# Kernel tuning notes

Measured on AMD Instinct MI355X. Metric: run time of the kernel, lower is better.

## Reference

```python
import jax, jax.numpy as jnp
import numpy as np

B, L, DIM, H = 2, 2048, 1024, 16
HD = DIM // H  # 64
EPS = 1e-6
ROPE_THETA = 10000.0


def _rmsnorm(x, scale):
    # mean of squares in float32 as in torch (dtype=torch.float32)
    ms = jnp.mean(jnp.square(x.astype(jnp.float32)), axis=-1, keepdims=True)
    inv = jax.lax.rsqrt(ms + EPS).astype(x.dtype)
    return x * inv * scale.astype(x.dtype)


def _rope_cos_sin(seq_len, head_dim, dtype):
    inv_freq = 1.0 / (ROPE_THETA ** (jnp.arange(0, head_dim, 2, dtype=jnp.float32) / head_dim))
    ang = jnp.arange(seq_len, dtype=jnp.float32)[:, None] * inv_freq[None, :]  # [L, HD/2]
    cos = jnp.cos(ang)[:, None, :].astype(dtype)  # [L,1,HD/2] broadcast over heads
    sin = jnp.sin(ang)[:, None, :].astype(dtype)
    return cos, sin


def _rope_apply(x, cos, sin):
    # x: [B,L,H,HD]; rotate-half formulation
    x1, x2 = jnp.split(x, 2, axis=-1)
    return jnp.concatenate([x1 * cos - x2 * sin, x2 * cos + x1 * sin], axis=-1)


def setup_inputs() -> dict:
    key = jax.random.key(0)
    k1, k2, k3 = jax.random.split(key, 3)
    x = jax.random.normal(k1, (B, L, DIM), dtype=jnp.float32)
    Wqkv = jax.random.normal(k2, (DIM, 3 * DIM), dtype=jnp.float32) * (DIM ** -0.5)
    Wproj = jax.random.normal(k3, (DIM, DIM), dtype=jnp.float32) * (DIM ** -0.5)
    q_scale = jnp.ones((HD,), dtype=jnp.float32)
    k_scale = jnp.ones((HD,), dtype=jnp.float32)
    bproj = jnp.zeros((DIM,), dtype=jnp.float32)
    return {"x": x, "Wqkv": Wqkv, "q_scale": q_scale, "k_scale": k_scale,
            "Wproj": Wproj, "bproj": bproj}


def reference(x, Wqkv, q_scale, k_scale, Wproj, bproj):
    b, l, c = x.shape
    qkv = x @ Wqkv  # [B,L,3*DIM]
    qkv = qkv.reshape(b, l, 3, H, HD)
    q, k, v = qkv[:, :, 0], qkv[:, :, 1], qkv[:, :, 2]  # each [B,L,H,HD]
    q = _rmsnorm(q, q_scale)
    k = _rmsnorm(k, k_scale)
    cos, sin = _rope_cos_sin(l, HD, x.dtype)
    q = _rope_apply(q, cos, sin)
    k = _rope_apply(k, cos, sin)
    scale = HD ** -0.5
    scores = jnp.einsum('blhd,bmhd->bhlm', q, k) * scale  # [B,H,L,L]
    p = jax.nn.softmax(scores, axis=-1)
    o = jnp.einsum('bhlm,bmhd->blhd', p, v).reshape(b, l, c)
    return o @ Wproj + bproj
```

## Files before the change

kernel.cpp:

```cpp
#include <hip/hip_runtime.h>
#include <hip/hip_bf16.h>
#include <cstdint>

#define B_   2
#define L_   2048
#define DIM_ 1024
#define H_   16
#define HD_  64
#define M_   (B_ * L_)
#define N3_  (3 * DIM_)

typedef unsigned short ushort_t;
typedef __bf16 bf16x8 __attribute__((ext_vector_type(8)));
typedef float  f32x4  __attribute__((ext_vector_type(4)));
typedef float  f32x16 __attribute__((ext_vector_type(16)));
typedef unsigned u32x2_t __attribute__((ext_vector_type(2)));

__device__ __forceinline__ unsigned short f2b(float f) {
  return __builtin_bit_cast(unsigned short, (__bf16)f);
}
__device__ __forceinline__ float b2f(unsigned short s) {
  unsigned u = ((unsigned)s) << 16;
  return __builtin_bit_cast(float, u);
}
__device__ __forceinline__ float fmax3(float a, float b, float c) {
  return fmaxf(fmaxf(a, b), c);
}

__device__ __forceinline__ void plswap(unsigned &a, unsigned &b) {
#if defined(__has_builtin) && __has_builtin(__builtin_amdgcn_permlane32_swap)
  u32x2_t r = __builtin_amdgcn_permlane32_swap(a, b, false, false);
  a = r[0]; b = r[1];
#else
  unsigned sa = (unsigned)__shfl_xor((int)a, 32);
  unsigned sb = (unsigned)__shfl_xor((int)b, 32);
  bool hi = (threadIdx.x & 32) != 0;
  unsigned na = hi ? sb : a;
  unsigned nb = hi ? b : sa;
  a = na; b = nb;
#endif
}

typedef const __attribute__((address_space(1))) void* as1cp;
typedef __attribute__((address_space(3))) void* as3p;
__device__ __forceinline__ void gload_lds16(const void* g, void* l) {
  __builtin_amdgcn_global_load_lds((as1cp)g, (as3p)l, 16, 0, 0);
}

__global__ __launch_bounds__(256)
void conv_bf16(const float* __restrict__ in, ushort_t* __restrict__ out, int n4) {
  int i = blockIdx.x * 256 + threadIdx.x;
  if (i >= n4) return;
  float4 v = *(const float4*)&in[(size_t)i * 4];
  ushort4 o;
  o.x = f2b(v.x); o.y = f2b(v.y); o.z = f2b(v.z); o.w = f2b(v.w);
  *(ushort4*)&out[(size_t)i * 4] = o;
}

__global__ __launch_bounds__(256)
void transpose_conv(const float* __restrict__ in, ushort_t* __restrict__ out,
                    int R, int C) {
  __shared__ float tile[64][65];
  const int t = threadIdx.x;
  const int r0 = blockIdx.y * 64, c0 = blockIdx.x * 64;
#pragma unroll
  for (int p = 0; p < 4; ++p) {
    int r = (t >> 4) + p * 16;
    int c = (t & 15) * 4;
    float4 v = *(const float4*)&in[(size_t)(r0 + r) * C + (c0 + c)];
    tile[r][c + 0] = v.x; tile[r][c + 1] = v.y;
    tile[r][c + 2] = v.z; tile[r][c + 3] = v.w;
  }
  __syncthreads();
#pragma unroll
  for (int p = 0; p < 4; ++p) {
    int cc = (t >> 4) + p * 16;
    int r  = (t & 15) * 4;
    ushort4 o;
    o.x = f2b(tile[r + 0][cc]); o.y = f2b(tile[r + 1][cc]);
    o.z = f2b(tile[r + 2][cc]); o.w = f2b(tile[r + 3][cc]);
    *(ushort4*)&out[(size_t)(c0 + cc) * R + (r0 + r)] = o;
  }
}

__global__ __launch_bounds__(256)
void rope_tab(float* __restrict__ cosT, float* __restrict__ sinT) {
  int idx = blockIdx.x * 256 + threadIdx.x;
  int l = idx >> 5, d = idx & 31;
  float inv_freq = expf(-((float)(2 * d) / 64.f) * logf(10000.f));
  float ang = (float)l * inv_freq;
  cosT[idx] = cosf(ang);
  sinT[idx] = sinf(ang);
}

template <int MODE>
__global__ __launch_bounds__(256)
void gemm_bt(const ushort_t* __restrict__ A, const ushort_t* __restrict__ BT,
             void* __restrict__ Cout, ushort_t* __restrict__ vtout,
             const float* __restrict__ bias, int M, int N, int K, int ldc) {
  __shared__ ushort_t As[128 * 32];
  __shared__ ushort_t Bs[128 * 32];
  const int lane = threadIdx.x & 63;
  const int wid  = threadIdx.x >> 6;
  const int wm = wid >> 1, wn = wid & 1;
  const int m0 = blockIdx.y * 128, n0 = blockIdx.x * 128;
  const int ro = lane & 15, kg = lane >> 4;

  f32x4 acc[4][4] = {};

  for (int k0 = 0; k0 < K; k0 += 32) {
    const int cb = wid * 128;
#pragma unroll
    for (int j = 0; j < 2; ++j) {
      int c = cb + j * 64 + lane;
      gload_lds16(A + (size_t)(m0 + (c >> 2)) * K + k0 + (c & 3) * 8,
                  &As[(cb + j * 64) * 8]);
    }
#pragma unroll
    for (int j = 0; j < 2; ++j) {
      int c = cb + j * 64 + lane;
      gload_lds16(BT + (size_t)(n0 + (c >> 2)) * K + k0 + (c & 3) * 8,
                  &Bs[(cb + j * 64) * 8]);
    }
    __syncthreads();
    bf16x8 af[4], bfr[4];
#pragma unroll
    for (int i = 0; i < 4; ++i)
      af[i] = *(const bf16x8*)&As[(wm * 64 + i * 16 + ro) * 32 + kg * 8];
#pragma unroll
    for (int i = 0; i < 4; ++i)
      bfr[i] = *(const bf16x8*)&Bs[(wn * 64 + i * 16 + ro) * 32 + kg * 8];
#pragma unroll
    for (int i = 0; i < 4; ++i)
#pragma unroll
      for (int j = 0; j < 4; ++j)
        acc[i][j] = __builtin_amdgcn_mfma_f32_16x16x32_bf16(af[i], bfr[j],
                                                            acc[i][j], 0, 0, 0);
    __syncthreads();
  }

  if (MODE == 0) {
    if (n0 < 2048) {
#pragma unroll
      for (int i = 0; i < 4; ++i)
#pragma unroll
        for (int r = 0; r < 4; ++r) {
          int row = m0 + wm * 64 + i * 16 + kg * 4 + r;
#pragma unroll
          for (int j = 0; j < 4; ++j) {
            int col = n0 + wn * 64 + j * 16 + ro;
            ((ushort_t*)Cout)[(size_t)row * ldc + col] = f2b(acc[i][j][r]);
          }
        }
    } else {
#pragma unroll
      for (int i = 0; i < 4; ++i) {
        int rowb = m0 + wm * 64 + i * 16 + kg * 4;
        int bb = rowb >> 11, l = rowb & (L_ - 1);
#pragma unroll
        for (int j = 0; j < 4; ++j) {
          int dg = (n0 - 2048) + wn * 64 + j * 16 + ro;
          ushort4 o;
          o.x = f2b(acc[i][j][0]); o.y = f2b(acc[i][j][1]);
          o.z = f2b(acc[i][j][2]); o.w = f2b(acc[i][j][3]);
          *(ushort4*)&vtout[((size_t)bb * DIM_ + dg) * L_ + l] = o;
        }
      }
    }
  } else {
#pragma unroll
    for (int i = 0; i < 4; ++i)
#pragma unroll
      for (int r = 0; r < 4; ++r) {
        int row = m0 + wm * 64 + i * 16 + kg * 4 + r;
#pragma unroll
        for (int j = 0; j < 4; ++j) {
          int col = n0 + wn * 64 + j * 16 + ro;
          ((float*)Cout)[(size_t)row * ldc + col] = acc[i][j][r] + bias[col];
        }
      }
  }
}

__global__ __launch_bounds__(256)
void rmsrope(ushort_t* __restrict__ qk, const float* __restrict__ qs,
             const float* __restrict__ ks, const float* __restrict__ cosT,
             const float* __restrict__ sinT) {
  const int t = blockIdx.x;
  const int l = t & (L_ - 1);
  const int j = threadIdx.x & 15;
  const int h = threadIdx.x >> 4;
  const int dd = (j & 7) * 4;
  float4 cv = *(const float4*)&cosT[l * 32 + dd];
  float4 sv = *(const float4*)&sinT[l * 32 + dd];
  const float sgn = (j < 8) ? -1.f : 1.f;
#pragma unroll
  for (int ic = 0; ic < 2; ++ic) {
    const float qsc = (ic == 0) ? 0.125f * 1.44269504088896341f : 1.f;
    ushort_t* base = qk + (size_t)t * 2048 + ic * DIM_ + h * HD_ + j * 4;
    ushort4 raw = *(const ushort4*)base;
    float x0 = b2f(raw.x), x1 = b2f(raw.y), x2 = b2f(raw.z), x3 = b2f(raw.w);
    float ss = x0 * x0 + x1 * x1 + x2 * x2 + x3 * x3;
    ss += __shfl_xor(ss, 1); ss += __shfl_xor(ss, 2);
    ss += __shfl_xor(ss, 4); ss += __shfl_xor(ss, 8);
    float inv = rsqrtf(ss * (1.f / 64.f) + 1e-6f);
    const float* scp = (ic == 0 ? qs : ks) + j * 4;
    float4 sc = *(const float4*)scp;
    x0 *= inv * sc.x; x1 *= inv * sc.y; x2 *= inv * sc.z; x3 *= inv * sc.w;
    float y0 = __shfl_xor(x0, 8), y1 = __shfl_xor(x1, 8);
    float y2 = __shfl_xor(x2, 8), y3 = __shfl_xor(x3, 8);
    ushort4 o;
    o.x = f2b((x0 * cv.x + sgn * y0 * sv.x) * qsc);
    o.y = f2b((x1 * cv.y + sgn * y1 * sv.y) * qsc);
    o.z = f2b((x2 * cv.z + sgn * y2 * sv.z) * qsc);
    o.w = f2b((x3 * cv.w + sgn * y3 * sv.w) * qsc);
    *(ushort4*)base = o;
  }
}

__global__ __launch_bounds__(256)
void flash_attn(const ushort_t* __restrict__ qk, const ushort_t* __restrict__ vt,
                ushort_t* __restrict__ O) {
  const int qt = blockIdx.x, h = blockIdx.y, b = blockIdx.z;
  const int lane = threadIdx.x & 63, wid = threadIdx.x >> 6;
  const int lq = lane & 31;
  const int hi = lane >> 5;
  const int q0 = qt * 128;
  const size_t tok0 = (size_t)b * L_;
  const ushort_t* qb = qk + tok0 * 2048 + h * HD_;
  const ushort_t* kb = qb + DIM_;
  const ushort_t* vb = vt + ((size_t)b * DIM_ + h * HD_) * L_;

  __shared__ ushort_t Ks[2][4096];
  __shared__ ushort_t Vs[2][4096];

  const int srow0 = wid * 16 + (lane >> 3);
  const int sch   = lane & 7;
  auto STAGE = [&](int bufi, int kt) {
#pragma unroll
    for (int j = 0; j < 2; ++j) {
      int row = srow0 + j * 8;
      int sc  = sch ^ (row & 7);
      gload_lds16(kb + (size_t)(kt * 64 + row) * 2048 + sc * 8,
                  &Ks[bufi][wid * 1024 + j * 512]);
      gload_lds16(vb + (size_t)row * L_ + kt * 64 + sc * 8,
                  &Vs[bufi][wid * 1024 + j * 512]);
    }
  };

  bf16x8 qf[4];
  {
    const ushort_t* gp = qb + (size_t)(q0 + wid * 32 + lq) * 2048;
#pragma unroll
    for (int s = 0; s < 4; ++s)
      qf[s] = *(const bf16x8*)(gp + s * 16 + hi * 8);
  }

  int chs[4];
#pragma unroll
  for (int s = 0; s < 4; ++s) chs[s] = ((2 * s + hi) ^ (lq & 7)) * 8;

  f32x16 oaccT[2] = {};
  float mrow = -1e30f, lrow = 0.f;

  STAGE(0, 0);
  __syncthreads();

  auto TILE = [&](int bi, int kt) {
    if (kt + 1 < L_ / 64) STAGE(bi ^ 1, kt + 1);
    const ushort_t* kb0 = &Ks[bi][lq * 64];
    const ushort_t* vb0 = &Vs[bi][lq * 64];

    f32x16 st[2];
    __builtin_amdgcn_s_setprio(1);
#pragma unroll
    for (int t = 0; t < 2; ++t) {
      f32x16 z = {};
#pragma unroll
      for (int s = 0; s < 4; ++s) {
        bf16x8 kf = *(const bf16x8*)(kb0 + t * 2048 + chs[s]);
        z = __builtin_amdgcn_mfma_f32_32x32x16_bf16(kf, qf[s], z, 0, 0, 0);
      }
      st[t] = z;
    }
    __builtin_amdgcn_s_setprio(0);

    float mx0, mx1, mx2, mx3;
    {
      float a0 = fmaxf(fmaxf(st[0][0], st[0][1]),  fmaxf(st[0][2], st[0][3]));
      float a1 = fmaxf(fmaxf(st[0][4], st[0][5]),  fmaxf(st[0][6], st[0][7]));
      float a2 = fmaxf(fmaxf(st[0][8], st[0][9]),  fmaxf(st[0][10], st[0][11]));
      float a3 = fmaxf(fmaxf(st[0][12], st[0][13]), fmaxf(st[0][14], st[0][15]));
      float b0 = fmaxf(fmaxf(st[1][0], st[1][1]),  fmaxf(st[1][2], st[1][3]));
      float b1 = fmaxf(fmaxf(st[1][4], st[1][5]),  fmaxf(st[1][6], st[1][7]));
      float b2 = fmaxf(fmaxf(st[1][8], st[1][9]),  fmaxf(st[1][10], st[1][11]));
      float b3 = fmaxf(fmaxf(st[1][12], st[1][13]), fmaxf(st[1][14], st[1][15]));
      mx0 = fmaxf(a0, b0); mx1 = fmaxf(a1, b1);
      mx2 = fmaxf(a2, b2); mx3 = fmaxf(a3, b3);
    }
    float pmw = fmaxf(fmax3(mx0, mx1, mx2), mx3);
    float pm  = fmaxf(pmw, __shfl_xor(pmw, 32));

    if (__any(pm > mrow + 8.f)) {
      float mn = fmaxf(mrow, pm);
      float alpha = __builtin_amdgcn_exp2f(mrow - mn);
      mrow = mn;
      lrow *= alpha;
#pragma unroll
      for (int dt = 0; dt < 2; ++dt)
#pragma unroll
        for (int r = 0; r < 16; ++r) oaccT[dt][r] *= alpha;
    }

    unsigned pk[2][8];
    float rs0 = 0.f, rs1 = 0.f, rs2 = 0.f, rs3 = 0.f;
#pragma unroll
    for (int t = 0; t < 2; ++t)
#pragma unroll
      for (int p = 0; p < 8; ++p) {
        float e0 = __builtin_amdgcn_exp2f(st[t][2 * p]     - mrow);
        float e1 = __builtin_amdgcn_exp2f(st[t][2 * p + 1] - mrow);
        if ((p & 3) == 0) { rs0 += e0; rs1 += e1; }
        else if ((p & 3) == 1) { rs2 += e0; rs3 += e1; }
        else if ((p & 3) == 2) { rs0 += e0; rs1 += e1; }
        else { rs2 += e0; rs3 += e1; }
        pk[t][p] = (unsigned)f2b(e0) | ((unsigned)f2b(e1) << 16);
      }
    lrow += (rs0 + rs1) + (rs2 + rs3);

    __builtin_amdgcn_s_setprio(1);
#pragma unroll
    for (int t = 0; t < 2; ++t)
#pragma unroll
      for (int blk = 0; blk < 2; ++blk) {
        unsigned w0 = pk[t][4 * blk + 0], w1 = pk[t][4 * blk + 1];
        unsigned w2 = pk[t][4 * blk + 2], w3 = pk[t][4 * blk + 3];
        plswap(w0, w2);
        plswap(w1, w3);
        uint4 bw; bw.x = w0; bw.y = w1; bw.z = w2; bw.w = w3;
        bf16x8 pf = __builtin_bit_cast(bf16x8, bw);
        const int sg = 2 * t + blk;
#pragma unroll
        for (int dt = 0; dt < 2; ++dt) {
          bf16x8 vf = *(const bf16x8*)(vb0 + dt * 2048 + chs[sg]);
          oaccT[dt] = __builtin_amdgcn_mfma_f32_32x32x16_bf16(vf, pf,
                                                              oaccT[dt], 0, 0, 0);
        }
      }
    __builtin_amdgcn_s_setprio(0);

    __syncthreads();
  };

  for (int kt = 0; kt < L_ / 64; kt += 2) {
    TILE(0, kt);
    TILE(1, kt + 1);
  }

  lrow += __shfl_xor(lrow, 32);
  float linv = 1.f / lrow;
  ushort_t* obp = O + (size_t)(tok0 + q0 + wid * 32 + lq) * DIM_ + h * HD_;
#pragma unroll
  for (int dt = 0; dt < 2; ++dt)
#pragma unroll
    for (int g4 = 0; g4 < 4; ++g4) {
      int d0 = dt * 32 + g4 * 8 + hi * 4;
      ushort4 o4;
      o4.x = f2b(oaccT[dt][4 * g4 + 0] * linv);
      o4.y = f2b(oaccT[dt][4 * g4 + 1] * linv);
      o4.z = f2b(oaccT[dt][4 * g4 + 2] * linv);
      o4.w = f2b(oaccT[dt][4 * g4 + 3] * linv);
      *(ushort4*)(obp + d0) = o4;
    }
}

extern "C" void kernel_launch(void* const* d_in, const int* in_sizes, int n_in,
                              void* d_out, int out_size, void* d_ws, size_t ws_size,
                              hipStream_t stream) {
  const float* x     = (const float*)d_in[0];
  const float* Wqkv  = (const float*)d_in[1];
  const float* qs    = (const float*)d_in[2];
  const float* ks    = (const float*)d_in[3];
  const float* Wproj = (const float*)d_in[4];
  const float* bproj = (const float*)d_in[5];
  float* out = (float*)d_out;

  char* ws = (char*)d_ws;
  ushort_t* xb     = (ushort_t*)(ws);
  ushort_t* WqkvT  = (ushort_t*)(ws + (size_t)(8u << 20));
  ushort_t* WprojT = (ushort_t*)(ws + (size_t)(14u << 20));
  ushort_t* qkb    = (ushort_t*)(ws + (size_t)(16u << 20));
  ushort_t* vtb    = (ushort_t*)(ws + (size_t)(32u << 20));
  float*    cosT   = (float*)(ws + (size_t)(40u << 20));
  float*    sinT   = (float*)(ws + (size_t)(40u << 20) + (256u << 10));
  ushort_t* ob     = (ushort_t*)(ws + (size_t)(41u << 20));

  conv_bf16<<<4096, 256, 0, stream>>>(x, xb, M_ * DIM_ / 4);
  transpose_conv<<<dim3(48, 16), 256, 0, stream>>>(Wqkv, WqkvT, DIM_, N3_);
  transpose_conv<<<dim3(16, 16), 256, 0, stream>>>(Wproj, WprojT, DIM_, DIM_);
  rope_tab<<<256, 256, 0, stream>>>(cosT, sinT);
  gemm_bt<0><<<dim3(24, 32), 256, 0, stream>>>(xb, WqkvT, qkb, vtb, nullptr,
                                               M_, N3_, DIM_, 2048);
  rmsrope<<<4096, 256, 0, stream>>>(qkb, qs, ks, cosT, sinT);
  flash_attn<<<dim3(16, 16, 2), 256, 0, stream>>>(qkb, vtb, ob);
  gemm_bt<1><<<dim3(8, 32), 256, 0, stream>>>(ob, WprojT, out, nullptr, bproj,
                                              M_, DIM_, DIM_, DIM_);
}
```

Before: 151.3 us.

## Split flash attention over KV halves with combine kernel and MFMA row sums

Flash attention now splits the key/value sequence into two halves via a SPLIT template, doubling the grid from 512 to 1024 blocks so more of the 256 CUs are busy. Each half writes fp32 partial outputs plus per-row max and sum to workspace, and a new attn_combine kernel merges them into the bf16 output. The softmax row sum is now accumulated with an extra MFMA against a ones vector rather than scalar adds, and the max reduction is restructured around fmax3. The cost is an extra launch and fp32 partial-output traffic, and the split path runs only when the workspace is large enough.

```diff
diff --git a/kernel.cpp b/kernel.cpp
--- a/kernel.cpp
+++ b/kernel.cpp
@@ -218,10 +218,16 @@
   }
 }
 
+template <int SPLIT>
 __global__ __launch_bounds__(256)
 void flash_attn(const ushort_t* __restrict__ qk, const ushort_t* __restrict__ vt,
-                ushort_t* __restrict__ O) {
-  const int qt = blockIdx.x, h = blockIdx.y, b = blockIdx.z;
+                ushort_t* __restrict__ O, float* __restrict__ Opart,
+                float* __restrict__ Ml) {
+  const int qt = blockIdx.x, h = blockIdx.y;
+  const int b  = SPLIT ? (int)(blockIdx.z >> 1) : (int)blockIdx.z;
+  const int ks = SPLIT ? (int)(blockIdx.z & 1) : 0;
+  const int ktBeg = SPLIT ? ks * (L_ / 128) : 0;
+  const int ktEnd = SPLIT ? ktBeg + (L_ / 128) : (L_ / 64);
   const int lane = threadIdx.x & 63, wid = threadIdx.x >> 6;
   const int lq = lane & 31;
   const int hi = lane >> 5;
@@ -256,18 +262,23 @@
       qf[s] = *(const bf16x8*)(gp + s * 16 + hi * 8);
   }
 
+  bf16x8 onesv;
+#pragma unroll
+  for (int i = 0; i < 8; ++i) onesv[i] = (__bf16)1.0f;
+
   int chs[4];
 #pragma unroll
   for (int s = 0; s < 4; ++s) chs[s] = ((2 * s + hi) ^ (lq & 7)) * 8;
 
   f32x16 oaccT[2] = {};
-  float mrow = -1e30f, lrow = 0.f;
-
-  STAGE(0, 0);
+  f32x16 laccv = {};
+  float mrow = -1e30f;
+
+  STAGE(0, ktBeg);
   __syncthreads();
 
   auto TILE = [&](int bi, int kt) {
-    if (kt + 1 < L_ / 64) STAGE(bi ^ 1, kt + 1);
+    if (kt + 1 < ktEnd) STAGE(bi ^ 1, kt + 1);
     const ushort_t* kb0 = &Ks[bi][lq * 64];
     const ushort_t* vb0 = &Vs[bi][lq * 64];
 
@@ -285,27 +296,29 @@
     }
     __builtin_amdgcn_s_setprio(0);
 
-    float mx0, mx1, mx2, mx3;
-    {
-      float a0 = fmaxf(fmaxf(st[0][0], st[0][1]),  fmaxf(st[0][2], st[0][3]));
-      float a1 = fmaxf(fmaxf(st[0][4], st[0][5]),  fmaxf(st[0][6], st[0][7]));
-      float a2 = fmaxf(fmaxf(st[0][8], st[0][9]),  fmaxf(st[0][10], st[0][11]));
-      float a3 = fmaxf(fmaxf(st[0][12], st[0][13]), fmaxf(st[0][14], st[0][15]));
-      float b0 = fmaxf(fmaxf(st[1][0], st[1][1]),  fmaxf(st[1][2], st[1][3]));
-      float b1 = fmaxf(fmaxf(st[1][4], st[1][5]),  fmaxf(st[1][6], st[1][7]));
-      float b2 = fmaxf(fmaxf(st[1][8], st[1][9]),  fmaxf(st[1][10], st[1][11]));
-      float b3 = fmaxf(fmaxf(st[1][12], st[1][13]), fmaxf(st[1][14], st[1][15]));
-      mx0 = fmaxf(a0, b0); mx1 = fmaxf(a1, b1);
-      mx2 = fmaxf(a2, b2); mx3 = fmaxf(a3, b3);
-    }
-    float pmw = fmaxf(fmax3(mx0, mx1, mx2), mx3);
+    float m01 = fmax3(st[0][0],  st[0][1],  st[0][2]);
+    float m02 = fmax3(st[0][3],  st[0][4],  st[0][5]);
+    float m03 = fmax3(st[0][6],  st[0][7],  st[0][8]);
+    float m04 = fmax3(st[0][9],  st[0][10], st[0][11]);
+    float m05 = fmax3(st[0][12], st[0][13], st[0][14]);
+    float m06 = fmax3(st[0][15], st[1][0],  st[1][1]);
+    float m07 = fmax3(st[1][2],  st[1][3],  st[1][4]);
+    float m08 = fmax3(st[1][5],  st[1][6],  st[1][7]);
+    float m09 = fmax3(st[1][8],  st[1][9],  st[1][10]);
+    float m10 = fmax3(st[1][11], st[1][12], st[1][13]);
+    float m11 = fmaxf(st[1][14], st[1][15]);
+    float n1 = fmax3(m01, m02, m03);
+    float n2 = fmax3(m04, m05, m06);
+    float n3 = fmax3(m07, m08, m09);
+    float n4 = fmax3(m10, m11, n1);
+    float pmw = fmax3(n2, n3, n4);
     float pm  = fmaxf(pmw, __shfl_xor(pmw, 32));
 
     if (__any(pm > mrow + 8.f)) {
       float mn = fmaxf(mrow, pm);
       float alpha = __builtin_amdgcn_exp2f(mrow - mn);
       mrow = mn;
-      lrow *= alpha;
+      laccv[0] *= alpha;
 #pragma unroll
       for (int dt = 0; dt < 2; ++dt)
 #pragma unroll
@@ -313,20 +326,14 @@
     }
 
     unsigned pk[2][8];
-    float rs0 = 0.f, rs1 = 0.f, rs2 = 0.f, rs3 = 0.f;
 #pragma unroll
     for (int t = 0; t < 2; ++t)
 #pragma unroll
       for (int p = 0; p < 8; ++p) {
         float e0 = __builtin_amdgcn_exp2f(st[t][2 * p]     - mrow);
         float e1 = __builtin_amdgcn_exp2f(st[t][2 * p + 1] - mrow);
-        if ((p & 3) == 0) { rs0 += e0; rs1 += e1; }
-        else if ((p & 3) == 1) { rs2 += e0; rs3 += e1; }
-        else if ((p & 3) == 2) { rs0 += e0; rs1 += e1; }
-        else { rs2 += e0; rs3 += e1; }
         pk[t][p] = (unsigned)f2b(e0) | ((unsigned)f2b(e1) << 16);
       }
-    lrow += (rs0 + rs1) + (rs2 + rs3);
 
     __builtin_amdgcn_s_setprio(1);
 #pragma unroll
@@ -340,6 +347,7 @@
         uint4 bw; bw.x = w0; bw.y = w1; bw.z = w2; bw.w = w3;
         bf16x8 pf = __builtin_bit_cast(bf16x8, bw);
         const int sg = 2 * t + blk;
+        laccv = __builtin_amdgcn_mfma_f32_32x32x16_bf16(onesv, pf, laccv, 0, 0, 0);
 #pragma unroll
         for (int dt = 0; dt < 2; ++dt) {
           bf16x8 vf = *(const bf16x8*)(vb0 + dt * 2048 + chs[sg]);
@@ -352,26 +360,72 @@
     __syncthreads();
   };
 
-  for (int kt = 0; kt < L_ / 64; kt += 2) {
+  for (int kt = ktBeg; kt < ktEnd; kt += 2) {
     TILE(0, kt);
     TILE(1, kt + 1);
   }
 
-  lrow += __shfl_xor(lrow, 32);
-  float linv = 1.f / lrow;
-  ushort_t* obp = O + (size_t)(tok0 + q0 + wid * 32 + lq) * DIM_ + h * HD_;
-#pragma unroll
-  for (int dt = 0; dt < 2; ++dt)
-#pragma unroll
-    for (int g4 = 0; g4 < 4; ++g4) {
-      int d0 = dt * 32 + g4 * 8 + hi * 4;
-      ushort4 o4;
-      o4.x = f2b(oaccT[dt][4 * g4 + 0] * linv);
-      o4.y = f2b(oaccT[dt][4 * g4 + 1] * linv);
-      o4.z = f2b(oaccT[dt][4 * g4 + 2] * linv);
-      o4.w = f2b(oaccT[dt][4 * g4 + 3] * linv);
-      *(ushort4*)(obp + d0) = o4;
-    }
+  const float linv = 1.f / laccv[0];
+  const int tok = (int)tok0 + q0 + wid * 32 + lq;
+  if (SPLIT) {
+    float* op = Opart + ((size_t)ks * M_ + tok) * DIM_ + h * HD_;
+#pragma unroll
+    for (int dt = 0; dt < 2; ++dt)
+#pragma unroll
+      for (int g4 = 0; g4 < 4; ++g4) {
+        int d0 = dt * 32 + g4 * 8 + hi * 4;
+        float4 o4;
+        o4.x = oaccT[dt][4 * g4 + 0] * linv;
+        o4.y = oaccT[dt][4 * g4 + 1] * linv;
+        o4.z = oaccT[dt][4 * g4 + 2] * linv;
+        o4.w = oaccT[dt][4 * g4 + 3] * linv;
+        *(float4*)(op + d0) = o4;
+      }
+    if (hi == 0) {
+      float2 ml; ml.x = mrow; ml.y = laccv[0];
+      *(float2*)&Ml[(((size_t)ks * M_ + tok) * H_ + h) * 2] = ml;
+    }
+  } else {
+    ushort_t* obp = O + (size_t)tok * DIM_ + h * HD_;
+#pragma unroll
+    for (int dt = 0; dt < 2; ++dt)
+#pragma unroll
+      for (int g4 = 0; g4 < 4; ++g4) {
+        int d0 = dt * 32 + g4 * 8 + hi * 4;
+        ushort4 o4;
+        o4.x = f2b(oaccT[dt][4 * g4 + 0] * linv);
+        o4.y = f2b(oaccT[dt][4 * g4 + 1] * linv);
+        o4.z = f2b(oaccT[dt][4 * g4 + 2] * linv);
+        o4.w = f2b(oaccT[dt][4 * g4 + 3] * linv);
+        *(ushort4*)(obp + d0) = o4;
+      }
+  }
+}
+
+__global__ __launch_bounds__(256)
+void attn_combine(const float* __restrict__ Opart, const float* __restrict__ Ml,
+                  ushort_t* __restrict__ O) {
+  int idx = blockIdx.x * 256 + threadIdx.x;
+  int dg  = idx & 15;
+  int rest = idx >> 4;
+  int h   = rest & 15;
+  int tok = rest >> 4;
+  float2 ml0 = *(const float2*)&Ml[(((size_t)0 * M_ + tok) * H_ + h) * 2];
+  float2 ml1 = *(const float2*)&Ml[(((size_t)1 * M_ + tok) * H_ + h) * 2];
+  float mM = fmaxf(ml0.x, ml1.x);
+  float w0 = ml0.y * __builtin_amdgcn_exp2f(ml0.x - mM);
+  float w1 = ml1.y * __builtin_amdgcn_exp2f(ml1.x - mM);
+  float inv = 1.f / (w0 + w1);
+  w0 *= inv; w1 *= inv;
+  size_t off = (size_t)tok * DIM_ + h * HD_ + dg * 4;
+  float4 a = *(const float4*)&Opart[off];
+  float4 c = *(const float4*)&Opart[(size_t)M_ * DIM_ + off];
+  ushort4 o;
+  o.x = f2b(a.x * w0 + c.x * w1);
+  o.y = f2b(a.y * w0 + c.y * w1);
+  o.z = f2b(a.z * w0 + c.z * w1);
+  o.w = f2b(a.w * w0 + c.w * w1);
+  *(ushort4*)&O[off] = o;
 }
 
 extern "C" void kernel_launch(void* const* d_in, const int* in_sizes, int n_in,
@@ -394,6 +448,8 @@
   float*    cosT   = (float*)(ws + (size_t)(40u << 20));
   float*    sinT   = (float*)(ws + (size_t)(40u << 20) + (256u << 10));
   ushort_t* ob     = (ushort_t*)(ws + (size_t)(41u << 20));
+  float*    Opart  = (float*)(ws + (size_t)(49u << 20));
+  float*    Ml     = (float*)(ws + (size_t)(81u << 20));
 
   conv_bf16<<<4096, 256, 0, stream>>>(x, xb, M_ * DIM_ / 4);
   transpose_conv<<<dim3(48, 16), 256, 0, stream>>>(Wqkv, WqkvT, DIM_, N3_);
@@ -402,7 +458,14 @@
   gemm_bt<0><<<dim3(24, 32), 256, 0, stream>>>(xb, WqkvT, qkb, vtb, nullptr,
                                                M_, N3_, DIM_, 2048);
   rmsrope<<<4096, 256, 0, stream>>>(qkb, qs, ks, cosT, sinT);
-  flash_attn<<<dim3(16, 16, 2), 256, 0, stream>>>(qkb, vtb, ob);
+  if (ws_size >= ((size_t)83u << 20)) {
+    flash_attn<1><<<dim3(16, 16, 4), 256, 0, stream>>>(qkb, vtb, nullptr,
+                                                       Opart, Ml);
+    attn_combine<<<4096, 256, 0, stream>>>(Opart, Ml, ob);
+  } else {
+    flash_attn<0><<<dim3(16, 16, 2), 256, 0, stream>>>(qkb, vtb, ob,
+                                                       nullptr, nullptr);
+  }
   gemm_bt<1><<<dim3(8, 32), 256, 0, stream>>>(ob, WprojT, out, nullptr, bproj,
                                               M_, DIM_, DIM_, DIM_);
 }
```

Result: slower. 159.8 us (+5.6%).

## Split attention KV range across two blocks and merge with combine kernel

Applied to the files above, without the earlier changes.

Flash attention gains a split-K template mode. Each of two blocks per query tile covers half of the key sequence and writes partial bf16 outputs plus running max/sum, and a new combine kernel merges the two halves with softmax rescaling. This doubles the grid from 512 to 1024 blocks to improve CU occupancy (with a launch-bounds hint of 3 blocks/CU). The inner tile loop is also restructured to process each 32-key subtile separately, folding the max subtraction into the MFMA accumulator init and using incremental pointer staging. The cost is an extra kernel launch, extra global traffic for the partials, and added bf16 rounding of the partial outputs. The split path is taken only when the workspace is large enough.

```diff
diff --git a/kernel.cpp b/kernel.cpp
--- a/kernel.cpp
+++ b/kernel.cpp
@@ -218,10 +218,16 @@
   }
 }
 
-__global__ __launch_bounds__(256)
+template <int SPLIT>
+__global__ __launch_bounds__(256, 3)
 void flash_attn(const ushort_t* __restrict__ qk, const ushort_t* __restrict__ vt,
-                ushort_t* __restrict__ O) {
-  const int qt = blockIdx.x, h = blockIdx.y, b = blockIdx.z;
+                ushort_t* __restrict__ O, ushort_t* __restrict__ Opart,
+                float* __restrict__ Ml) {
+  const int qt = blockIdx.x, h = blockIdx.y;
+  const int b  = SPLIT ? (int)(blockIdx.z >> 1) : (int)blockIdx.z;
+  const int ks = SPLIT ? (int)(blockIdx.z & 1) : 0;
+  const int ktBeg = SPLIT ? ks * (L_ / 128) : 0;
+  const int ktEnd = SPLIT ? ktBeg + (L_ / 128) : (L_ / 64);
   const int lane = threadIdx.x & 63, wid = threadIdx.x >> 6;
   const int lq = lane & 31;
   const int hi = lane >> 5;
@@ -235,17 +241,16 @@
   __shared__ ushort_t Vs[2][4096];
 
   const int srow0 = wid * 16 + (lane >> 3);
-  const int sch   = lane & 7;
-  auto STAGE = [&](int bufi, int kt) {
-#pragma unroll
-    for (int j = 0; j < 2; ++j) {
-      int row = srow0 + j * 8;
-      int sc  = sch ^ (row & 7);
-      gload_lds16(kb + (size_t)(kt * 64 + row) * 2048 + sc * 8,
-                  &Ks[bufi][wid * 1024 + j * 512]);
-      gload_lds16(vb + (size_t)row * L_ + kt * 64 + sc * 8,
-                  &Vs[bufi][wid * 1024 + j * 512]);
-    }
+  const int sc    = (lane & 7) ^ (srow0 & 7);
+  const ushort_t* kst = kb + (size_t)(ktBeg * 64 + srow0) * 2048 + sc * 8;
+  const ushort_t* vst = vb + (size_t)srow0 * L_ + ktBeg * 64 + sc * 8;
+  auto STAGE = [&](int bufi) {
+    gload_lds16(kst,            &Ks[bufi][wid * 1024]);
+    gload_lds16(kst + 8 * 2048, &Ks[bufi][wid * 1024 + 512]);
+    gload_lds16(vst,            &Vs[bufi][wid * 1024]);
+    gload_lds16(vst + 8 * L_,   &Vs[bufi][wid * 1024 + 512]);
+    kst += 64 * 2048;
+    vst += 64;
   };
 
   bf16x8 qf[4];
@@ -261,80 +266,68 @@
   for (int s = 0; s < 4; ++s) chs[s] = ((2 * s + hi) ^ (lq & 7)) * 8;
 
   f32x16 oaccT[2] = {};
-  float mrow = -1e30f, lrow = 0.f;
-
-  STAGE(0, 0);
+  float mrow = 0.f;
+  float lrow = 0.f;
+
+  STAGE(0);
   __syncthreads();
 
-  auto TILE = [&](int bi, int kt) {
-    if (kt + 1 < L_ / 64) STAGE(bi ^ 1, kt + 1);
+  auto TILE = [&](int bi, bool more) {
+    if (more) STAGE(bi ^ 1);
     const ushort_t* kb0 = &Ks[bi][lq * 64];
     const ushort_t* vb0 = &Vs[bi][lq * 64];
-
-    f32x16 st[2];
-    __builtin_amdgcn_s_setprio(1);
 #pragma unroll
     for (int t = 0; t < 2; ++t) {
-      f32x16 z = {};
+      f32x16 st;
+#pragma unroll
+      for (int i = 0; i < 16; ++i) st[i] = -mrow;
+      __builtin_amdgcn_s_setprio(1);
 #pragma unroll
       for (int s = 0; s < 4; ++s) {
         bf16x8 kf = *(const bf16x8*)(kb0 + t * 2048 + chs[s]);
-        z = __builtin_amdgcn_mfma_f32_32x32x16_bf16(kf, qf[s], z, 0, 0, 0);
-      }
-      st[t] = z;
-    }
-    __builtin_amdgcn_s_setprio(0);
-
-    float mx0, mx1, mx2, mx3;
-    {
-      float a0 = fmaxf(fmaxf(st[0][0], st[0][1]),  fmaxf(st[0][2], st[0][3]));
-      float a1 = fmaxf(fmaxf(st[0][4], st[0][5]),  fmaxf(st[0][6], st[0][7]));
-      float a2 = fmaxf(fmaxf(st[0][8], st[0][9]),  fmaxf(st[0][10], st[0][11]));
-      float a3 = fmaxf(fmaxf(st[0][12], st[0][13]), fmaxf(st[0][14], st[0][15]));
-      float b0 = fmaxf(fmaxf(st[1][0], st[1][1]),  fmaxf(st[1][2], st[1][3]));
-      float b1 = fmaxf(fmaxf(st[1][4], st[1][5]),  fmaxf(st[1][6], st[1][7]));
-      float b2 = fmaxf(fmaxf(st[1][8], st[1][9]),  fmaxf(st[1][10], st[1][11]));
-      float b3 = fmaxf(fmaxf(st[1][12], st[1][13]), fmaxf(st[1][14], st[1][15]));
-      mx0 = fmaxf(a0, b0); mx1 = fmaxf(a1, b1);
-      mx2 = fmaxf(a2, b2); mx3 = fmaxf(a3, b3);
-    }
-    float pmw = fmaxf(fmax3(mx0, mx1, mx2), mx3);
-    float pm  = fmaxf(pmw, __shfl_xor(pmw, 32));
-
-    if (__any(pm > mrow + 8.f)) {
-      float mn = fmaxf(mrow, pm);
-      float alpha = __builtin_amdgcn_exp2f(mrow - mn);
-      mrow = mn;
-      lrow *= alpha;
-#pragma unroll
-      for (int dt = 0; dt < 2; ++dt)
-#pragma unroll
-        for (int r = 0; r < 16; ++r) oaccT[dt][r] *= alpha;
-    }
-
-    unsigned pk[2][8];
-    float rs0 = 0.f, rs1 = 0.f, rs2 = 0.f, rs3 = 0.f;
-#pragma unroll
-    for (int t = 0; t < 2; ++t)
+        st = __builtin_amdgcn_mfma_f32_32x32x16_bf16(kf, qf[s], st, 0, 0, 0);
+      }
+      __builtin_amdgcn_s_setprio(0);
+
+      float m1 = fmax3(st[0],  st[1],  st[2]);
+      float m2 = fmax3(st[3],  st[4],  st[5]);
+      float m3 = fmax3(st[6],  st[7],  st[8]);
+      float m4 = fmax3(st[9],  st[10], st[11]);
+      float m5 = fmax3(st[12], st[13], st[14]);
+      float n1 = fmax3(m1, m2, st[15]);
+      float n2 = fmax3(m3, m4, m5);
+      float pm = fmaxf(n1, n2);
+      pm = fmaxf(pm, __shfl_xor(pm, 32));
+
+      if (__any(pm > 8.f)) {
+        float d = fmaxf(pm, 0.f);
+        float alpha = __builtin_amdgcn_exp2f(-d);
+        mrow += d;
+        lrow *= alpha;
+#pragma unroll
+        for (int dt = 0; dt < 2; ++dt)
+#pragma unroll
+          for (int r = 0; r < 16; ++r) oaccT[dt][r] *= alpha;
+#pragma unroll
+        for (int i = 0; i < 16; ++i) st[i] -= d;
+      }
+
+      unsigned pk[8];
+      float rs0 = 0.f, rs1 = 0.f;
 #pragma unroll
       for (int p = 0; p < 8; ++p) {
-        float e0 = __builtin_amdgcn_exp2f(st[t][2 * p]     - mrow);
-        float e1 = __builtin_amdgcn_exp2f(st[t][2 * p + 1] - mrow);
-        if ((p & 3) == 0) { rs0 += e0; rs1 += e1; }
-        else if ((p & 3) == 1) { rs2 += e0; rs3 += e1; }
-        else if ((p & 3) == 2) { rs0 += e0; rs1 += e1; }
-        else { rs2 += e0; rs3 += e1; }
-        pk[t][p] = (unsigned)f2b(e0) | ((unsigned)f2b(e1) << 16);
-      }
-    lrow += (rs0 + rs1) + (rs2 + rs3);
-
-    __builtin_amdgcn_s_setprio(1);
-#pragma unroll
-    for (int t = 0; t < 2; ++t)
+        float e0 = __builtin_amdgcn_exp2f(st[2 * p]);
+        float e1 = __builtin_amdgcn_exp2f(st[2 * p + 1]);
+        rs0 += e0; rs1 += e1;
+        pk[p] = (unsigned)f2b(e0) | ((unsigned)f2b(e1) << 16);
+      }
+      lrow += rs0 + rs1;
+
+      __builtin_amdgcn_s_setprio(1);
 #pragma unroll
       for (int blk = 0; blk < 2; ++blk) {
-        unsigned w0 = pk[t][4 * blk + 0], w1 = pk[t][4 * blk + 1];
-        unsigned w2 = pk[t][4 * blk + 2], w3 = pk[t][4 * blk + 3];
+        unsigned w0 = pk[4 * blk + 0], w1 = pk[4 * blk + 1];
+        unsigned w2 = pk[4 * blk + 2], w3 = pk[4 * blk + 3];
         plswap(w0, w2);
         plswap(w1, w3);
         uint4 bw; bw.x = w0; bw.y = w1; bw.z = w2; bw.w = w3;
@@ -347,19 +340,22 @@
                                                               oaccT[dt], 0, 0, 0);
         }
       }
-    __builtin_amdgcn_s_setprio(0);
-
+      __builtin_amdgcn_s_setprio(0);
+    }
     __syncthreads();
   };
 
-  for (int kt = 0; kt < L_ / 64; kt += 2) {
-    TILE(0, kt);
-    TILE(1, kt + 1);
+  const int NT = ktEnd - ktBeg;
+  for (int it = 0; it < NT; it += 2) {
+    TILE(0, it + 1 < NT);
+    TILE(1, it + 2 < NT);
   }
 
   lrow += __shfl_xor(lrow, 32);
-  float linv = 1.f / lrow;
-  ushort_t* obp = O + (size_t)(tok0 + q0 + wid * 32 + lq) * DIM_ + h * HD_;
+  const float linv = 1.f / lrow;
+  const int tok = (int)tok0 + q0 + wid * 32 + lq;
+  ushort_t* obp = (SPLIT ? Opart + (size_t)ks * M_ * DIM_ : O)
+                  + (size_t)tok * DIM_ + h * HD_;
 #pragma unroll
   for (int dt = 0; dt < 2; ++dt)
 #pragma unroll
@@ -372,6 +368,39 @@
       o4.w = f2b(oaccT[dt][4 * g4 + 3] * linv);
       *(ushort4*)(obp + d0) = o4;
     }
+  if (SPLIT && hi == 0) {
+    float2 ml; ml.x = mrow; ml.y = lrow;
+    *(float2*)&Ml[(((size_t)ks * M_ + tok) * H_ + h) * 2] = ml;
+  }
+}
+
+__global__ __launch_bounds__(256)
+void attn_combine(const ushort_t* __restrict__ Opart, const float* __restrict__ Ml,
+                  ushort_t* __restrict__ O) {
+  int idx = blockIdx.x * 256 + threadIdx.x;
+  int c   = idx & 127;
+  int tok = idx >> 7;
+  int h   = c >> 3;
+  float2 ml0 = *(const float2*)&Ml[(((size_t)0 * M_ + tok) * H_ + h) * 2];
+  float2 ml1 = *(const float2*)&Ml[(((size_t)1 * M_ + tok) * H_ + h) * 2];
+  float mM = fmaxf(ml0.x, ml1.x);
+  float w0 = ml0.y * __builtin_amdgcn_exp2f(ml0.x - mM);
+  float w1 = ml1.y * __builtin_amdgcn_exp2f(ml1.x - mM);
+  float inv = 1.f / (w0 + w1);
+  w0 *= inv; w1 *= inv;
+  size_t off = (size_t)tok * DIM_ + c * 8;
+  uint4 a = *(const uint4*)&Opart[off];
+  uint4 d = *(const uint4*)&Opart[(size_t)M_ * DIM_ + off];
+  auto mix = [&](unsigned ua, unsigned ud) -> unsigned {
+    float a0 = b2f((unsigned short)(ua & 0xffff)), a1 = b2f((unsigned short)(ua >> 16));
+    float d0 = b2f((unsigned short)(ud & 0xffff)), d1 = b2f((unsigned short)(ud >> 16));
+    unsigned r0 = f2b(a0 * w0 + d0 * w1), r1 = f2b(a1 * w0 + d1 * w1);
+    return r0 | (r1 << 16);
+  };
+  uint4 o;
+  o.x = mix(a.x, d.x); o.y = mix(a.y, d.y);
+  o.z = mix(a.z, d.z); o.w = mix(a.w, d.w);
+  *(uint4*)&O[off] = o;
 }
 
 extern "C" void kernel_launch(void* const* d_in, const int* in_sizes, int n_in,
@@ -394,6 +423,8 @@
   float*    cosT   = (float*)(ws + (size_t)(40u << 20));
   float*    sinT   = (float*)(ws + (size_t)(40u << 20) + (256u << 10));
   ushort_t* ob     = (ushort_t*)(ws + (size_t)(41u << 20));
+  ushort_t* Opart  = (ushort_t*)(ws + (size_t)(49u << 20));
+  float*    Ml     = (float*)(ws + (size_t)(65u << 20));
 
   conv_bf16<<<4096, 256, 0, stream>>>(x, xb, M_ * DIM_ / 4);
   transpose_conv<<<dim3(48, 16), 256, 0, stream>>>(Wqkv, WqkvT, DIM_, N3_);
@@ -402,7 +433,14 @@
   gemm_bt<0><<<dim3(24, 32), 256, 0, stream>>>(xb, WqkvT, qkb, vtb, nullptr,
                                                M_, N3_, DIM_, 2048);
   rmsrope<<<4096, 256, 0, stream>>>(qkb, qs, ks, cosT, sinT);
-  flash_attn<<<dim3(16, 16, 2), 256, 0, stream>>>(qkb, vtb, ob);
+  if (ws_size >= ((size_t)66u << 20)) {
+    flash_attn<1><<<dim3(16, 16, 4), 256, 0, stream>>>(qkb, vtb, nullptr,
+                                                       Opart, Ml);
+    attn_combine<<<2048, 256, 0, stream>>>(Opart, Ml, ob);
+  } else {
+    flash_attn<0><<<dim3(16, 16, 2), 256, 0, stream>>>(qkb, vtb, ob,
+                                                       nullptr, nullptr);
+  }
   gemm_bt<1><<<dim3(8, 32), 256, 0, stream>>>(ob, WprojT, out, nullptr, bproj,
                                               M_, DIM_, DIM_, DIM_);
 }
```

Measured after the change: 152.7 us. No clear change (+0.9%).
